# Performance work log

Hardware: AMD Instinct MI355X
Metric: run time of the kernel (lower is better)

Reference implementation:

```python
import jax, jax.numpy as jnp
import numpy as np

ANCHORS = [[[116, 90], [156, 198], [373, 326]], [[30, 61], [62, 45], [59, 119]], [[10, 13], [16, 30], [33, 23]]]
INPUT_SIZE = 416.0
B, G, C = 32, 20, 80


def _decode_scale(inp, anch):
    # inp: [B, 3*(5+C), W, W]
    Bq, _, W, _ = inp.shape
    sf = INPUT_SIZE / W
    p = inp.reshape(Bq, 3, -1, W, W).transpose(0, 1, 3, 4, 2)  # [B,3,W,W,5+C]
    sx = jax.nn.sigmoid(p[..., 0])
    sy = jax.nn.sigmoid(p[..., 1])
    w = p[..., 2]
    h = p[..., 3]
    conf = jax.nn.sigmoid(p[..., 4])
    cls = jax.nn.sigmoid(p[..., 5:])
    gx = jnp.arange(W, dtype=inp.dtype)[None, None, None, :]  # varies along cols
    gy = jnp.arange(W, dtype=inp.dtype)[None, None, :, None]  # varies along rows
    a = jnp.floor(jnp.asarray(anch, dtype=inp.dtype) / sf)  # // scale_factor as in source
    aw = a[:, 0][None, :, None, None]
    ah = a[:, 1][None, :, None, None]
    bx = (sx + gx) * sf
    by = (sy + gy) * sf
    bw = jnp.exp(w) * aw * sf
    bh = jnp.exp(h) * ah * sf
    out = jnp.concatenate([bx[..., None], by[..., None], bw[..., None], bh[..., None], conf[..., None], cls], axis=-1)
    return out.reshape(Bq, -1, 5 + cls.shape[-1])  # [B, 3*W*W, 5+C]


def _forward(x0, x1, x2, batch_y):
    xs = [x0, x1, x2]
    Bq = x0.shape[0]
    img_dim = x0.shape[1] // 3
    w1 = x0.shape[-1]  # source uses width1 for ALL scales (faithful bug reproduction)
    raw = jnp.concatenate(
        [xi.reshape(Bq, 3, -1, w1, w1).transpose(0, 1, 3, 4, 2).reshape(Bq, -1, img_dim) for xi in xs], axis=1)
    dec = jnp.concatenate([_decode_scale(xi, ANCHORS[i]) for i, xi in enumerate(xs)], axis=1)  # [B,N,5+C]
    # pairwise IoU between every decoded box [B,1,N] and every GT [B,G,1]
    pb = dec[..., :4]
    px, py, pw, ph = pb[..., 0][:, None, :], pb[..., 1][:, None, :], pb[..., 2][:, None, :], pb[..., 3][:, None, :]
    gb = batch_y[..., :4]
    gxc, gyc, gw, gh = gb[..., 0][..., None], gb[..., 1][..., None], gb[..., 2][..., None], gb[..., 3][..., None]
    xl = jnp.maximum(px, gxc)
    yt = jnp.maximum(py, gyc)
    xr = jnp.minimum(px + pw, gxc + gw)
    yb = jnp.minimum(py + ph, gyc + gh)
    inter = jnp.clip(xr - xl, 0) * jnp.clip(yb - yt, 0)
    iou = inter / (pw * ph + gw * gh - inter)  # [B,G,N]
    pos = jnp.argmax(iou, axis=-1)  # [B,G] (first max, like torch.max)
    neg_mask = (iou < 0.5).astype(dec.dtype)  # [B,G,N]
    x_pos = jnp.take_along_axis(raw[..., :4], pos[..., None], axis=1)  # [B,G,4]
    conf = dec[..., 4]  # [B,N]
    conf_pos = jnp.take_along_axis(conf, pos, axis=1)  # [B,G]
    cls_pos = jnp.take_along_axis(dec[..., 5:], pos[..., None], axis=1)  # [B,G,C]
    labels = batch_y[..., 4].astype(jnp.int32)  # [B,G]
    mse = jnp.mean((x_pos - gb) ** 2, axis=-1)  # MSELoss on the single matched row
    obj = jnp.log(conf_pos + 1e-9)
    log1m = jnp.log(1.0 - conf + 1e-9)[:, None, :]  # [B,1,N]
    cnt = jnp.maximum(jnp.sum(neg_mask, axis=-1), 1.0)
    noobj = jnp.sum(neg_mask * log1m, axis=-1) / cnt  # masked mean over negatives
    ce = -jnp.take_along_axis(jax.nn.log_softmax(cls_pos, axis=-1), labels[..., None], axis=-1)[..., 0]
    # loss += box*MSE - obj*mean(log conf) - noobj*mean(log(1-conf)) - class*CE  (rates all 1)
    return jnp.sum(1.0 * mse - 1.0 * obj - 1.0 * noobj - 1.0 * ce)


def setup_inputs() -> dict:
    key = jax.random.key(0)
    k0, k1, k2, k3, k4, k5 = jax.random.split(key, 6)
    ch = 3 * (5 + C)
    x0 = jax.random.normal(k0, (B, ch, 13, 13), dtype=jnp.float32)
    x1 = jax.random.normal(k1, (B, ch, 26, 26), dtype=jnp.float32)
    x2 = jax.random.normal(k2, (B, ch, 52, 52), dtype=jnp.float32)
    xy = jax.random.uniform(k3, (B, G, 2), dtype=jnp.float32) * 350.0
    wh = jax.random.uniform(k4, (B, G, 2), dtype=jnp.float32) * 90.0 + 10.0
    lab = jax.random.randint(k5, (B, G, 1), 0, C).astype(jnp.float32)
    batch_y = jnp.concatenate([xy, wh, lab], axis=-1)  # [B,G,5]: x,y,w,h,class
    return {"x0": x0, "x1": x1, "x2": x2, "batch_y": batch_y}


def reference(x0, x1, x2, batch_y):
    return _forward(x0, x1, x2, batch_y)
```

## Files before the change

kernel.cpp:

```cpp
#include <hip/hip_runtime.h>


constexpr int B_ = 32;
constexpr int G_ = 20;
constexpr int C_ = 80;

__global__ void zero_out_kernel(float* __restrict__ out) {
    out[0] = 0.0f;
}

__device__ __forceinline__ float sigm(float x) { return 1.0f / (1.0f + expf(-x)); }

template <int W, int NBASE>
__device__ __forceinline__ void scan_scale(
    const float* __restrict__ x, int b, float sf,
    float aw0, float aw1, float aw2, float ah0, float ah1, float ah2,
    float gxc, float gyc, float gx2, float gy2, float garea,
    float& best_iou, int& best_idx, float& neg_sum, float& neg_cnt)
{
    constexpr int WW = W * W;
    constexpr int NS = 3 * WW;
    for (int i = threadIdx.x; i < NS; i += 256) {
        int a   = i / WW;
        int rem = i - a * WW;
        int y   = rem / W;
        int xi  = rem - y * W;
        const float* base = x + (size_t)(b * 255 + a * 85) * WW + rem;
        float p0 = base[0];
        float p1 = base[WW];
        float p2 = base[2 * WW];
        float p3 = base[3 * WW];
        float p4 = base[4 * WW];
        float aw = (a == 0) ? aw0 : ((a == 1) ? aw1 : aw2);
        float ah = (a == 0) ? ah0 : ((a == 1) ? ah1 : ah2);
        float px = (sigm(p0) + (float)xi) * sf;
        float py = (sigm(p1) + (float)y) * sf;
        float pw = expf(p2) * aw;
        float ph = expf(p3) * ah;
        float conf = sigm(p4);
        float xl = fmaxf(px, gxc);
        float yt = fmaxf(py, gyc);
        float xr = fminf(px + pw, gx2);
        float yb = fminf(py + ph, gy2);
        float inter = fmaxf(xr - xl, 0.0f) * fmaxf(yb - yt, 0.0f);
        float iou = inter / (pw * ph + garea - inter);
        if (iou > best_iou) { best_iou = iou; best_idx = NBASE + i; }
        if (iou < 0.5f) { neg_sum += logf(1.0f - conf + 1e-9f); neg_cnt += 1.0f; }
    }
}

__global__ __launch_bounds__(256) void yolo_loss_kernel(
    const float* __restrict__ x0, const float* __restrict__ x1,
    const float* __restrict__ x2, const float* __restrict__ by,
    float* __restrict__ out)
{
    const int g = blockIdx.x;
    const int b = blockIdx.y;
    const float* yrow = by + (size_t)(b * G_ + g) * 5;
    const float gxc = yrow[0], gyc = yrow[1], gw = yrow[2], gh = yrow[3];
    const int label = (int)yrow[4];
    const float gx2 = gxc + gw, gy2 = gyc + gh, garea = gw * gh;

    float best_iou = -1e30f;
    int best_idx = 0x7fffffff;
    float neg_sum = 0.0f, neg_cnt = 0.0f;

    scan_scale<13, 0>(x0, b, 32.0f, 96.0f, 128.0f, 352.0f, 64.0f, 192.0f, 320.0f,
                      gxc, gyc, gx2, gy2, garea, best_iou, best_idx, neg_sum, neg_cnt);
    scan_scale<26, 507>(x1, b, 16.0f, 16.0f, 48.0f, 48.0f, 48.0f, 32.0f, 112.0f,
                        gxc, gyc, gx2, gy2, garea, best_iou, best_idx, neg_sum, neg_cnt);
    scan_scale<52, 2535>(x2, b, 8.0f, 8.0f, 16.0f, 32.0f, 8.0f, 24.0f, 16.0f,
                         gxc, gyc, gx2, gy2, garea, best_iou, best_idx, neg_sum, neg_cnt);

    for (int off = 32; off > 0; off >>= 1) {
        float oi  = __shfl_down(best_iou, off);
        int   oix = __shfl_down(best_idx, off);
        float ons = __shfl_down(neg_sum, off);
        float onc = __shfl_down(neg_cnt, off);
        if (oi > best_iou || (oi == best_iou && oix < best_idx)) { best_iou = oi; best_idx = oix; }
        neg_sum += ons;
        neg_cnt += onc;
    }

    __shared__ float s_iou[4];
    __shared__ int   s_idx[4];
    __shared__ float s_ns[4], s_nc[4];
    const int wave = threadIdx.x >> 6;
    const int lane = threadIdx.x & 63;
    if (lane == 0) { s_iou[wave] = best_iou; s_idx[wave] = best_idx; s_ns[wave] = neg_sum; s_nc[wave] = neg_cnt; }
    __syncthreads();

    if (threadIdx.x < 64) {
        float biou = (lane < 4) ? s_iou[lane] : -1e30f;
        int   bidx = (lane < 4) ? s_idx[lane] : 0x7fffffff;
        float ns   = (lane < 4) ? s_ns[lane] : 0.0f;
        float nc   = (lane < 4) ? s_nc[lane] : 0.0f;
        for (int off = 2; off > 0; off >>= 1) {
            float oi  = __shfl_xor(biou, off);
            int   oix = __shfl_xor(bidx, off);
            float ons = __shfl_xor(ns, off);
            float onc = __shfl_xor(nc, off);
            if (oi > biou || (oi == biou && oix < bidx)) { biou = oi; bidx = oix; }
            ns += ons;
            nc += onc;
        }
        const int pos = __shfl(bidx, 0);

        const float* xp;
        int local, WWv;
        if (pos < 507)        { xp = x0; local = pos;        WWv = 169;  }
        else if (pos < 2535)  { xp = x1; local = pos - 507;  WWv = 676;  }
        else                  { xp = x2; local = pos - 2535; WWv = 2704; }
        const int a   = local / WWv;
        const int rem = local - a * WWv;
        const float* basep = xp + (size_t)(b * 255 + a * 85) * WWv + rem;

        float s0v = sigm(basep[(5 + lane) * WWv]);
        float s1v = -1e30f;
        if (lane < C_ - 64) s1v = sigm(basep[(5 + 64 + lane) * WWv]);
        float m = fmaxf(s0v, s1v);
        for (int off = 32; off > 0; off >>= 1) m = fmaxf(m, __shfl_xor(m, off));
        float e = expf(s0v - m) + ((lane < C_ - 64) ? expf(s1v - m) : 0.0f);
        for (int off = 32; off > 0; off >>= 1) e += __shfl_xor(e, off);

        if (lane == 0) {
            float vl = sigm(basep[(5 + label) * WWv]);
            float ce = -(vl - m - logf(e));

            float r0 = basep[0];
            float r1 = basep[WWv];
            float r2 = basep[2 * WWv];
            float r3 = basep[3 * WWv];
            float d0 = r0 - gxc, d1 = r1 - gyc, d2 = r2 - gw, d3 = r3 - gh;
            float mse = 0.25f * (d0 * d0 + d1 * d1 + d2 * d2 + d3 * d3);

            float confp = sigm(basep[4 * WWv]);
            float obj = logf(confp + 1e-9f);
            float noobj = ns / fmaxf(nc, 1.0f);

            atomicAdd(out, mse - obj - noobj - ce);
        }
    }
}

extern "C" void kernel_launch(void* const* d_in, const int* in_sizes, int n_in,
                              void* d_out, int out_size, void* d_ws, size_t ws_size,
                              hipStream_t stream) {
    const float* x0 = (const float*)d_in[0];
    const float* x1 = (const float*)d_in[1];
    const float* x2 = (const float*)d_in[2];
    const float* by = (const float*)d_in[3];
    float* out = (float*)d_out;

    hipLaunchKernelGGL(zero_out_kernel, dim3(1), dim3(1), 0, stream, out);
    dim3 grid(G_, B_);
    hipLaunchKernelGGL(yolo_loss_kernel, grid, dim3(256), 0, stream,
                       x0, x1, x2, by, out);
}
```

Baseline: 181.4 us.

## Precompute decoded boxes once per batch and reuse across GT scans

Adds a decode kernel that computes box corners, area and log(1-conf) once per anchor per batch and writes them to workspace, plus a per-batch total of log1m. The scan kernel then reads the precomputed float4 pairs instead of redoing sigmoid/exp/log for every GT. The negative sum is obtained as the total minus the positive sum, which removes the per-GT log. The scan blocks are also remapped so that one batch's GTs share an XCD for L2 reuse. The cost is extra kernel launches and a workspace write and read of about 11 MB. The original path is kept as a fallback when the workspace is too small.

New measurement: 164.9 us. -9.1%, faster.

```diff
diff --git a/kernel.cpp b/kernel.cpp
--- a/kernel.cpp
+++ b/kernel.cpp
@@ -4,15 +4,202 @@
 constexpr int B_ = 32;
 constexpr int G_ = 20;
 constexpr int C_ = 80;
-
-__global__ void zero_out_kernel(float* __restrict__ out) {
-    out[0] = 0.0f;
-}
+constexpr int N_ = 10647;
+
+constexpr size_t DEC_BYTES = (size_t)B_ * N_ * 2 * sizeof(float4);
+constexpr size_t WS_NEEDED = DEC_BYTES + B_ * sizeof(float);
 
 __device__ __forceinline__ float sigm(float x) { return 1.0f / (1.0f + expf(-x)); }
 
+__global__ void init_kernel(float* __restrict__ tot, float* __restrict__ out) {
+    int t = threadIdx.x;
+    if (t < B_) tot[t] = 0.0f;
+    if (t == 0) out[0] = 0.0f;
+}
+
 template <int W, int NBASE>
-__device__ __forceinline__ void scan_scale(
+__device__ __forceinline__ void decode_scale(
+    const float* __restrict__ x, int b, int n, float sf,
+    float aw0, float aw1, float aw2, float ah0, float ah1, float ah2,
+    float4& d0, float4& d1)
+{
+    constexpr int WW = W * W;
+    int local = n - NBASE;
+    int a   = local / WW;
+    int rem = local - a * WW;
+    int y   = rem / W;
+    int xi  = rem - y * W;
+    const float* base = x + (size_t)(b * 255 + a * 85) * WW + rem;
+    float p0 = base[0];
+    float p1 = base[WW];
+    float p2 = base[2 * WW];
+    float p3 = base[3 * WW];
+    float p4 = base[4 * WW];
+    float aw = (a == 0) ? aw0 : ((a == 1) ? aw1 : aw2);
+    float ah = (a == 0) ? ah0 : ((a == 1) ? ah1 : ah2);
+    float px = (sigm(p0) + (float)xi) * sf;
+    float py = (sigm(p1) + (float)y) * sf;
+    float pw = expf(p2) * aw;
+    float ph = expf(p3) * ah;
+    float conf  = sigm(p4);
+    float log1m = logf(1.0f - conf + 1e-9f);
+    d0 = make_float4(px, py, px + pw, py + ph);
+    d1 = make_float4(pw * ph, log1m, 0.0f, 0.0f);
+}
+
+__global__ __launch_bounds__(256) void decode_kernel(
+    const float* __restrict__ x0, const float* __restrict__ x1,
+    const float* __restrict__ x2,
+    float4* __restrict__ dec, float* __restrict__ tot)
+{
+    const int b = blockIdx.y;
+    const int base = blockIdx.x * 1024;
+    float lsum = 0.0f;
+    for (int k = 0; k < 4; ++k) {
+        int n = base + k * 256 + threadIdx.x;
+        if (n < N_) {
+            float4 d0, d1;
+            if (n < 507)
+                decode_scale<13, 0>(x0, b, n, 32.0f, 96.0f, 128.0f, 352.0f,
+                                    64.0f, 192.0f, 320.0f, d0, d1);
+            else if (n < 2535)
+                decode_scale<26, 507>(x1, b, n, 16.0f, 16.0f, 48.0f, 48.0f,
+                                      48.0f, 32.0f, 112.0f, d0, d1);
+            else
+                decode_scale<52, 2535>(x2, b, n, 8.0f, 8.0f, 16.0f, 32.0f,
+                                       8.0f, 24.0f, 16.0f, d0, d1);
+            lsum += d1.y;
+            size_t o = ((size_t)b * N_ + n) * 2;
+            dec[o]     = d0;
+            dec[o + 1] = d1;
+        }
+    }
+    for (int off = 32; off > 0; off >>= 1) lsum += __shfl_down(lsum, off);
+    __shared__ float s_sum[4];
+    const int wave = threadIdx.x >> 6;
+    const int lane = threadIdx.x & 63;
+    if (lane == 0) s_sum[wave] = lsum;
+    __syncthreads();
+    if (threadIdx.x == 0)
+        atomicAdd(&tot[b], s_sum[0] + s_sum[1] + s_sum[2] + s_sum[3]);
+}
+
+__global__ __launch_bounds__(256) void scan_kernel(
+    const float* __restrict__ x0, const float* __restrict__ x1,
+    const float* __restrict__ x2,
+    const float4* __restrict__ dec, const float* __restrict__ by,
+    const float* __restrict__ tot, float* __restrict__ out)
+{
+    const int id   = blockIdx.x;
+    const int xcd  = id & 7;
+    const int slot = id >> 3;
+    const int q    = slot / 20;
+    const int b    = xcd * 4 + q;
+    const int g    = slot - q * 20;
+
+    const float* yrow = by + (size_t)(b * G_ + g) * 5;
+    const float gxc = yrow[0], gyc = yrow[1], gw = yrow[2], gh = yrow[3];
+    const int label = (int)yrow[4];
+    const float gx2 = gxc + gw, gy2 = gyc + gh, garea = gw * gh;
+
+    const float4* dp = dec + (size_t)b * N_ * 2;
+
+    float best_iou = -1.0f;
+    int best_idx = 0x7fffffff;
+    float pos_sum = 0.0f, pos_cnt = 0.0f;
+
+    for (int n = threadIdx.x; n < N_; n += 256) {
+        float4 d0 = dp[2 * n];
+        float4 d1 = dp[2 * n + 1];
+        float xl = fmaxf(d0.x, gxc);
+        float yt = fmaxf(d0.y, gyc);
+        float xr = fminf(d0.z, gx2);
+        float yb = fminf(d0.w, gy2);
+        float inter = fmaxf(xr - xl, 0.0f) * fmaxf(yb - yt, 0.0f);
+        float u = d1.x + garea - inter;
+        float iou = inter / u;
+        if (iou > best_iou) { best_iou = iou; best_idx = n; }
+        if (iou >= 0.5f) { pos_sum += d1.y; pos_cnt += 1.0f; }
+    }
+
+    for (int off = 32; off > 0; off >>= 1) {
+        float oi  = __shfl_down(best_iou, off);
+        int   oix = __shfl_down(best_idx, off);
+        float ops = __shfl_down(pos_sum, off);
+        float opc = __shfl_down(pos_cnt, off);
+        if (oi > best_iou || (oi == best_iou && oix < best_idx)) { best_iou = oi; best_idx = oix; }
+        pos_sum += ops;
+        pos_cnt += opc;
+    }
+
+    __shared__ float s_iou[4];
+    __shared__ int   s_idx[4];
+    __shared__ float s_ps[4], s_pc[4];
+    const int wave = threadIdx.x >> 6;
+    const int lane = threadIdx.x & 63;
+    if (lane == 0) { s_iou[wave] = best_iou; s_idx[wave] = best_idx; s_ps[wave] = pos_sum; s_pc[wave] = pos_cnt; }
+    __syncthreads();
+
+    if (threadIdx.x < 64) {
+        float biou = (lane < 4) ? s_iou[lane] : -1.0f;
+        int   bidx = (lane < 4) ? s_idx[lane] : 0x7fffffff;
+        float ps   = (lane < 4) ? s_ps[lane] : 0.0f;
+        float pc   = (lane < 4) ? s_pc[lane] : 0.0f;
+        for (int off = 2; off > 0; off >>= 1) {
+            float oi  = __shfl_xor(biou, off);
+            int   oix = __shfl_xor(bidx, off);
+            float ops = __shfl_xor(ps, off);
+            float opc = __shfl_xor(pc, off);
+            if (oi > biou || (oi == biou && oix < bidx)) { biou = oi; bidx = oix; }
+            ps += ops;
+            pc += opc;
+        }
+        const int pos = __shfl(bidx, 0);
+
+        const float* xp;
+        int local, WWv;
+        if (pos < 507)        { xp = x0; local = pos;        WWv = 169;  }
+        else if (pos < 2535)  { xp = x1; local = pos - 507;  WWv = 676;  }
+        else                  { xp = x2; local = pos - 2535; WWv = 2704; }
+        const int a   = local / WWv;
+        const int rem = local - a * WWv;
+        const float* basep = xp + (size_t)(b * 255 + a * 85) * WWv + rem;
+
+        float s0v = sigm(basep[(5 + lane) * WWv]);
+        float s1v = -1e30f;
+        if (lane < C_ - 64) s1v = sigm(basep[(5 + 64 + lane) * WWv]);
+        float m = fmaxf(s0v, s1v);
+        for (int off = 32; off > 0; off >>= 1) m = fmaxf(m, __shfl_xor(m, off));
+        float e = expf(s0v - m) + ((lane < C_ - 64) ? expf(s1v - m) : 0.0f);
+        for (int off = 32; off > 0; off >>= 1) e += __shfl_xor(e, off);
+
+        if (lane == 0) {
+            float vl = sigm(basep[(5 + label) * WWv]);
+            float ce = -(vl - m - logf(e));
+
+            float r0 = basep[0];
+            float r1 = basep[WWv];
+            float r2 = basep[2 * WWv];
+            float r3 = basep[3 * WWv];
+            float d0 = r0 - gxc, d1 = r1 - gyc, d2 = r2 - gw, d3 = r3 - gh;
+            float mse = 0.25f * (d0 * d0 + d1 * d1 + d2 * d2 + d3 * d3);
+
+            float confp = sigm(basep[4 * WWv]);
+            float obj = logf(confp + 1e-9f);
+
+            float neg_sum = tot[b] - ps;
+            float neg_cnt = (float)N_ - pc;
+            float noobj = neg_sum / fmaxf(neg_cnt, 1.0f);
+
+            atomicAdd(out, mse - obj - noobj - ce);
+        }
+    }
+}
+
+__global__ void zero_out_kernel(float* __restrict__ out) { out[0] = 0.0f; }
+
+template <int W, int NBASE>
+__device__ __forceinline__ void scan_scale_fb(
     const float* __restrict__ x, int b, float sf,
     float aw0, float aw1, float aw2, float ah0, float ah1, float ah2,
     float gxc, float gyc, float gx2, float gy2, float garea,
@@ -26,11 +213,7 @@
         int y   = rem / W;
         int xi  = rem - y * W;
         const float* base = x + (size_t)(b * 255 + a * 85) * WW + rem;
-        float p0 = base[0];
-        float p1 = base[WW];
-        float p2 = base[2 * WW];
-        float p3 = base[3 * WW];
-        float p4 = base[4 * WW];
+        float p0 = base[0], p1 = base[WW], p2 = base[2 * WW], p3 = base[3 * WW], p4 = base[4 * WW];
         float aw = (a == 0) ? aw0 : ((a == 1) ? aw1 : aw2);
         float ah = (a == 0) ? ah0 : ((a == 1) ? ah1 : ah2);
         float px = (sigm(p0) + (float)xi) * sf;
@@ -38,10 +221,8 @@
         float pw = expf(p2) * aw;
         float ph = expf(p3) * ah;
         float conf = sigm(p4);
-        float xl = fmaxf(px, gxc);
-        float yt = fmaxf(py, gyc);
-        float xr = fminf(px + pw, gx2);
-        float yb = fminf(py + ph, gy2);
+        float xl = fmaxf(px, gxc), yt = fmaxf(py, gyc);
+        float xr = fminf(px + pw, gx2), yb = fminf(py + ph, gy2);
         float inter = fmaxf(xr - xl, 0.0f) * fmaxf(yb - yt, 0.0f);
         float iou = inter / (pw * ph + garea - inter);
         if (iou > best_iou) { best_iou = iou; best_idx = NBASE + i; }
@@ -49,7 +230,7 @@
     }
 }
 
-__global__ __launch_bounds__(256) void yolo_loss_kernel(
+__global__ __launch_bounds__(256) void yolo_loss_fallback(
     const float* __restrict__ x0, const float* __restrict__ x1,
     const float* __restrict__ x2, const float* __restrict__ by,
     float* __restrict__ out)
@@ -65,12 +246,12 @@
     int best_idx = 0x7fffffff;
     float neg_sum = 0.0f, neg_cnt = 0.0f;
 
-    scan_scale<13, 0>(x0, b, 32.0f, 96.0f, 128.0f, 352.0f, 64.0f, 192.0f, 320.0f,
-                      gxc, gyc, gx2, gy2, garea, best_iou, best_idx, neg_sum, neg_cnt);
-    scan_scale<26, 507>(x1, b, 16.0f, 16.0f, 48.0f, 48.0f, 48.0f, 32.0f, 112.0f,
-                        gxc, gyc, gx2, gy2, garea, best_iou, best_idx, neg_sum, neg_cnt);
-    scan_scale<52, 2535>(x2, b, 8.0f, 8.0f, 16.0f, 32.0f, 8.0f, 24.0f, 16.0f,
+    scan_scale_fb<13, 0>(x0, b, 32.0f, 96.0f, 128.0f, 352.0f, 64.0f, 192.0f, 320.0f,
                          gxc, gyc, gx2, gy2, garea, best_iou, best_idx, neg_sum, neg_cnt);
+    scan_scale_fb<26, 507>(x1, b, 16.0f, 16.0f, 48.0f, 48.0f, 48.0f, 32.0f, 112.0f,
+                           gxc, gyc, gx2, gy2, garea, best_iou, best_idx, neg_sum, neg_cnt);
+    scan_scale_fb<52, 2535>(x2, b, 8.0f, 8.0f, 16.0f, 32.0f, 8.0f, 24.0f, 16.0f,
+                            gxc, gyc, gx2, gy2, garea, best_iou, best_idx, neg_sum, neg_cnt);
 
     for (int off = 32; off > 0; off >>= 1) {
         float oi  = __shfl_down(best_iou, off);
@@ -126,18 +307,12 @@
         if (lane == 0) {
             float vl = sigm(basep[(5 + label) * WWv]);
             float ce = -(vl - m - logf(e));
-
-            float r0 = basep[0];
-            float r1 = basep[WWv];
-            float r2 = basep[2 * WWv];
-            float r3 = basep[3 * WWv];
+            float r0 = basep[0], r1 = basep[WWv], r2 = basep[2 * WWv], r3 = basep[3 * WWv];
             float d0 = r0 - gxc, d1 = r1 - gyc, d2 = r2 - gw, d3 = r3 - gh;
             float mse = 0.25f * (d0 * d0 + d1 * d1 + d2 * d2 + d3 * d3);
-
             float confp = sigm(basep[4 * WWv]);
             float obj = logf(confp + 1e-9f);
             float noobj = ns / fmaxf(nc, 1.0f);
-
             atomicAdd(out, mse - obj - noobj - ce);
         }
     }
@@ -152,8 +327,17 @@
     const float* by = (const float*)d_in[3];
     float* out = (float*)d_out;
 
-    hipLaunchKernelGGL(zero_out_kernel, dim3(1), dim3(1), 0, stream, out);
-    dim3 grid(G_, B_);
-    hipLaunchKernelGGL(yolo_loss_kernel, grid, dim3(256), 0, stream,
-                       x0, x1, x2, by, out);
-}
+    if (ws_size >= WS_NEEDED) {
+        float4* dec = (float4*)d_ws;
+        float*  tot = (float*)((char*)d_ws + DEC_BYTES);
+        hipLaunchKernelGGL(init_kernel, dim3(1), dim3(64), 0, stream, tot, out);
+        hipLaunchKernelGGL(decode_kernel, dim3(11, B_), dim3(256), 0, stream,
+                           x0, x1, x2, dec, tot);
+        hipLaunchKernelGGL(scan_kernel, dim3(B_ * G_), dim3(256), 0, stream,
+                           x0, x1, x2, dec, by, tot, out);
+    } else {
+        hipLaunchKernelGGL(zero_out_kernel, dim3(1), dim3(1), 0, stream, out);
+        hipLaunchKernelGGL(yolo_loss_fallback, dim3(G_, B_), dim3(256), 0, stream,
+                           x0, x1, x2, by, out);
+    }
+}
```

## Decode boxes once per batch chunk and reuse across all GT boxes

Applied to the files above, without the earlier changes.

Previously every (batch, GT) block re-decoded all 10647 predicted boxes with sigmoid/exp/log, repeating the decode G times per batch. Now blocks tile over prediction chunks, decode each box once into registers, and loop over the 20 GT boxes held in shared memory. Argmax is merged across blocks with a packed 64-bit atomicMax key, and the negative-log sum is computed as total minus the positive sum. A separate epilogue kernel computes the per-GT loss terms. This adds workspace atomics and an extra launch, and the grid becomes small (6x32 blocks).

After: 168.9 us. 1.07x faster.

```diff
diff --git a/kernel.cpp b/kernel.cpp
--- a/kernel.cpp
+++ b/kernel.cpp
@@ -4,142 +4,213 @@
 constexpr int B_ = 32;
 constexpr int G_ = 20;
 constexpr int C_ = 80;
-
-__global__ void zero_out_kernel(float* __restrict__ out) {
-    out[0] = 0.0f;
-}
+constexpr int N_ = 10647;
+constexpr int PPT = 8;
+constexpr int CHUNK = 256 * PPT;
+constexpr int NCHUNK = (N_ + CHUNK - 1) / CHUNK;
+
+constexpr size_t OFF_KEY = 0;
+constexpr size_t OFF_PS  = OFF_KEY + (size_t)B_ * G_ * 8;
+constexpr size_t OFF_PC  = OFF_PS  + (size_t)B_ * G_ * 4;
+constexpr size_t OFF_TOT = OFF_PC  + (size_t)B_ * G_ * 4;
+constexpr size_t WS_NEEDED = OFF_TOT + B_ * 4;
 
 __device__ __forceinline__ float sigm(float x) { return 1.0f / (1.0f + expf(-x)); }
 
+__global__ __launch_bounds__(256) void init_kernel(
+    unsigned long long* __restrict__ key, float* __restrict__ ps,
+    float* __restrict__ pc, float* __restrict__ tot, float* __restrict__ out)
+{
+    const int t = threadIdx.x;
+    for (int i = t; i < B_ * G_; i += 256) { key[i] = 0ull; ps[i] = 0.0f; pc[i] = 0.0f; }
+    if (t < B_) tot[t] = 0.0f;
+    if (t == 0) out[0] = 0.0f;
+}
+
 template <int W, int NBASE>
-__device__ __forceinline__ void scan_scale(
-    const float* __restrict__ x, int b, float sf,
+__device__ __forceinline__ void decode_scale(
+    const float* __restrict__ x, int b, int n, float sf,
     float aw0, float aw1, float aw2, float ah0, float ah1, float ah2,
-    float gxc, float gyc, float gx2, float gy2, float garea,
-    float& best_iou, int& best_idx, float& neg_sum, float& neg_cnt)
+    float& x1o, float& y1o, float& x2o, float& y2o, float& area, float& l1m)
 {
     constexpr int WW = W * W;
-    constexpr int NS = 3 * WW;
-    for (int i = threadIdx.x; i < NS; i += 256) {
-        int a   = i / WW;
-        int rem = i - a * WW;
-        int y   = rem / W;
-        int xi  = rem - y * W;
-        const float* base = x + (size_t)(b * 255 + a * 85) * WW + rem;
-        float p0 = base[0];
-        float p1 = base[WW];
-        float p2 = base[2 * WW];
-        float p3 = base[3 * WW];
-        float p4 = base[4 * WW];
-        float aw = (a == 0) ? aw0 : ((a == 1) ? aw1 : aw2);
-        float ah = (a == 0) ? ah0 : ((a == 1) ? ah1 : ah2);
-        float px = (sigm(p0) + (float)xi) * sf;
-        float py = (sigm(p1) + (float)y) * sf;
-        float pw = expf(p2) * aw;
-        float ph = expf(p3) * ah;
-        float conf = sigm(p4);
-        float xl = fmaxf(px, gxc);
-        float yt = fmaxf(py, gyc);
-        float xr = fminf(px + pw, gx2);
-        float yb = fminf(py + ph, gy2);
-        float inter = fmaxf(xr - xl, 0.0f) * fmaxf(yb - yt, 0.0f);
-        float iou = inter / (pw * ph + garea - inter);
-        if (iou > best_iou) { best_iou = iou; best_idx = NBASE + i; }
-        if (iou < 0.5f) { neg_sum += logf(1.0f - conf + 1e-9f); neg_cnt += 1.0f; }
-    }
-}
-
-__global__ __launch_bounds__(256) void yolo_loss_kernel(
+    int local = n - NBASE;
+    int a   = local / WW;
+    int rem = local - a * WW;
+    int y   = rem / W;
+    int xi  = rem - y * W;
+    const float* base = x + (size_t)(b * 255 + a * 85) * WW + rem;
+    float p0 = base[0];
+    float p1 = base[WW];
+    float p2 = base[2 * WW];
+    float p3 = base[3 * WW];
+    float p4 = base[4 * WW];
+    float aw = (a == 0) ? aw0 : ((a == 1) ? aw1 : aw2);
+    float ah = (a == 0) ? ah0 : ((a == 1) ? ah1 : ah2);
+    float px = (sigm(p0) + (float)xi) * sf;
+    float py = (sigm(p1) + (float)y) * sf;
+    float pw = expf(p2) * aw;
+    float ph = expf(p3) * ah;
+    float conf = sigm(p4);
+    x1o = px; y1o = py; x2o = px + pw; y2o = py + ph;
+    area = pw * ph;
+    l1m = logf(1.0f - conf + 1e-9f);
+}
+
+__global__ __launch_bounds__(256) void fused_kernel(
     const float* __restrict__ x0, const float* __restrict__ x1,
     const float* __restrict__ x2, const float* __restrict__ by,
+    unsigned long long* __restrict__ key, float* __restrict__ ps,
+    float* __restrict__ pc, float* __restrict__ tot)
+{
+    const int b    = blockIdx.y;
+    const int base = blockIdx.x * CHUNK;
+    const int tid  = threadIdx.x;
+
+    __shared__ float s_gt[G_][5];
+    __shared__ unsigned long long s_key[G_][4];
+    __shared__ float s_ps[G_][4], s_pc[G_][4], s_l1m[4];
+
+    if (tid < G_) {
+        const float* yr = by + (size_t)(b * G_ + tid) * 5;
+        float gxc = yr[0], gyc = yr[1], gw = yr[2], gh = yr[3];
+        s_gt[tid][0] = gxc; s_gt[tid][1] = gyc;
+        s_gt[tid][2] = gxc + gw; s_gt[tid][3] = gyc + gh;
+        s_gt[tid][4] = gw * gh;
+    }
+    __syncthreads();
+
+    float bx1[PPT], by1[PPT], bx2[PPT], by2[PPT], bar[PPT], bl1[PPT];
+    float lsum = 0.0f;
+    #pragma unroll
+    for (int k = 0; k < PPT; ++k) {
+        int n = base + k * 256 + tid;
+        float X1 = 0, Y1 = 0, X2 = 0, Y2 = 0, AR = 0, L1 = 0;
+        if (n < N_) {
+            if (n < 507)
+                decode_scale<13, 0>(x0, b, n, 32.0f, 96.0f, 128.0f, 352.0f,
+                                    64.0f, 192.0f, 320.0f, X1, Y1, X2, Y2, AR, L1);
+            else if (n < 2535)
+                decode_scale<26, 507>(x1, b, n, 16.0f, 16.0f, 48.0f, 48.0f,
+                                      48.0f, 32.0f, 112.0f, X1, Y1, X2, Y2, AR, L1);
+            else
+                decode_scale<52, 2535>(x2, b, n, 8.0f, 8.0f, 16.0f, 32.0f,
+                                       8.0f, 24.0f, 16.0f, X1, Y1, X2, Y2, AR, L1);
+        }
+        bx1[k] = X1; by1[k] = Y1; bx2[k] = X2; by2[k] = Y2; bar[k] = AR; bl1[k] = L1;
+        lsum += L1;
+    }
+
+    const int wave = tid >> 6;
+    const int lane = tid & 63;
+    for (int g = 0; g < G_; ++g) {
+        float gxc = s_gt[g][0], gyc = s_gt[g][1];
+        float gx2 = s_gt[g][2], gy2 = s_gt[g][3], garea = s_gt[g][4];
+        float bi = -1.0f; int bidx = 0x7FFFFFFF;
+        float lps = 0.0f, lpc = 0.0f;
+        #pragma unroll
+        for (int k = 0; k < PPT; ++k) {
+            float xl = fmaxf(bx1[k], gxc);
+            float yt = fmaxf(by1[k], gyc);
+            float xr = fminf(bx2[k], gx2);
+            float yb = fminf(by2[k], gy2);
+            float inter = fmaxf(xr - xl, 0.0f) * fmaxf(yb - yt, 0.0f);
+            float u = bar[k] + garea - inter;
+            float iou = inter / u;
+            int n = base + k * 256 + tid;
+            iou = (n < N_) ? iou : -1.0f;
+            if (iou > bi) { bi = iou; bidx = n; }
+            if (iou >= 0.5f) { lps += bl1[k]; lpc += 1.0f; }
+        }
+        unsigned long long kk = (bi < 0.0f) ? 0ull
+            : (((unsigned long long)__float_as_uint(bi) << 32)
+               | (unsigned)(0x7FFFFFFF - bidx));
+        for (int off = 32; off > 0; off >>= 1) {
+            unsigned long long ok = __shfl_down(kk, off);
+            float ops = __shfl_down(lps, off);
+            float opc = __shfl_down(lpc, off);
+            kk = (ok > kk) ? ok : kk;
+            lps += ops; lpc += opc;
+        }
+        if (lane == 0) { s_key[g][wave] = kk; s_ps[g][wave] = lps; s_pc[g][wave] = lpc; }
+    }
+
+    for (int off = 32; off > 0; off >>= 1) lsum += __shfl_down(lsum, off);
+    if (lane == 0) s_l1m[wave] = lsum;
+    __syncthreads();
+
+    if (tid < G_) {
+        unsigned long long kk = s_key[tid][0];
+        float lps = s_ps[tid][0], lpc = s_pc[tid][0];
+        #pragma unroll
+        for (int w = 1; w < 4; ++w) {
+            unsigned long long ok = s_key[tid][w];
+            kk = (ok > kk) ? ok : kk;
+            lps += s_ps[tid][w]; lpc += s_pc[tid][w];
+        }
+        const int idx = b * G_ + tid;
+        atomicMax(&key[idx], kk);
+        atomicAdd(&ps[idx], lps);
+        atomicAdd(&pc[idx], lpc);
+    }
+    if (tid == 0)
+        atomicAdd(&tot[b], s_l1m[0] + s_l1m[1] + s_l1m[2] + s_l1m[3]);
+}
+
+__global__ __launch_bounds__(64) void epilogue_kernel(
+    const float* __restrict__ x0, const float* __restrict__ x1,
+    const float* __restrict__ x2, const float* __restrict__ by,
+    const unsigned long long* __restrict__ key, const float* __restrict__ ps,
+    const float* __restrict__ pc, const float* __restrict__ tot,
     float* __restrict__ out)
 {
     const int g = blockIdx.x;
     const int b = blockIdx.y;
+    const int lane = threadIdx.x;
+
+    const unsigned long long kk = key[b * G_ + g];
+    const int pos = 0x7FFFFFFF - (int)(kk & 0xFFFFFFFFull);
+
     const float* yrow = by + (size_t)(b * G_ + g) * 5;
     const float gxc = yrow[0], gyc = yrow[1], gw = yrow[2], gh = yrow[3];
     const int label = (int)yrow[4];
-    const float gx2 = gxc + gw, gy2 = gyc + gh, garea = gw * gh;
-
-    float best_iou = -1e30f;
-    int best_idx = 0x7fffffff;
-    float neg_sum = 0.0f, neg_cnt = 0.0f;
-
-    scan_scale<13, 0>(x0, b, 32.0f, 96.0f, 128.0f, 352.0f, 64.0f, 192.0f, 320.0f,
-                      gxc, gyc, gx2, gy2, garea, best_iou, best_idx, neg_sum, neg_cnt);
-    scan_scale<26, 507>(x1, b, 16.0f, 16.0f, 48.0f, 48.0f, 48.0f, 32.0f, 112.0f,
-                        gxc, gyc, gx2, gy2, garea, best_iou, best_idx, neg_sum, neg_cnt);
-    scan_scale<52, 2535>(x2, b, 8.0f, 8.0f, 16.0f, 32.0f, 8.0f, 24.0f, 16.0f,
-                         gxc, gyc, gx2, gy2, garea, best_iou, best_idx, neg_sum, neg_cnt);
-
-    for (int off = 32; off > 0; off >>= 1) {
-        float oi  = __shfl_down(best_iou, off);
-        int   oix = __shfl_down(best_idx, off);
-        float ons = __shfl_down(neg_sum, off);
-        float onc = __shfl_down(neg_cnt, off);
-        if (oi > best_iou || (oi == best_iou && oix < best_idx)) { best_iou = oi; best_idx = oix; }
-        neg_sum += ons;
-        neg_cnt += onc;
-    }
-
-    __shared__ float s_iou[4];
-    __shared__ int   s_idx[4];
-    __shared__ float s_ns[4], s_nc[4];
-    const int wave = threadIdx.x >> 6;
-    const int lane = threadIdx.x & 63;
-    if (lane == 0) { s_iou[wave] = best_iou; s_idx[wave] = best_idx; s_ns[wave] = neg_sum; s_nc[wave] = neg_cnt; }
-    __syncthreads();
-
-    if (threadIdx.x < 64) {
-        float biou = (lane < 4) ? s_iou[lane] : -1e30f;
-        int   bidx = (lane < 4) ? s_idx[lane] : 0x7fffffff;
-        float ns   = (lane < 4) ? s_ns[lane] : 0.0f;
-        float nc   = (lane < 4) ? s_nc[lane] : 0.0f;
-        for (int off = 2; off > 0; off >>= 1) {
-            float oi  = __shfl_xor(biou, off);
-            int   oix = __shfl_xor(bidx, off);
-            float ons = __shfl_xor(ns, off);
-            float onc = __shfl_xor(nc, off);
-            if (oi > biou || (oi == biou && oix < bidx)) { biou = oi; bidx = oix; }
-            ns += ons;
-            nc += onc;
-        }
-        const int pos = __shfl(bidx, 0);
-
-        const float* xp;
-        int local, WWv;
-        if (pos < 507)        { xp = x0; local = pos;        WWv = 169;  }
-        else if (pos < 2535)  { xp = x1; local = pos - 507;  WWv = 676;  }
-        else                  { xp = x2; local = pos - 2535; WWv = 2704; }
-        const int a   = local / WWv;
-        const int rem = local - a * WWv;
-        const float* basep = xp + (size_t)(b * 255 + a * 85) * WWv + rem;
-
-        float s0v = sigm(basep[(5 + lane) * WWv]);
-        float s1v = -1e30f;
-        if (lane < C_ - 64) s1v = sigm(basep[(5 + 64 + lane) * WWv]);
-        float m = fmaxf(s0v, s1v);
-        for (int off = 32; off > 0; off >>= 1) m = fmaxf(m, __shfl_xor(m, off));
-        float e = expf(s0v - m) + ((lane < C_ - 64) ? expf(s1v - m) : 0.0f);
-        for (int off = 32; off > 0; off >>= 1) e += __shfl_xor(e, off);
-
-        if (lane == 0) {
-            float vl = sigm(basep[(5 + label) * WWv]);
-            float ce = -(vl - m - logf(e));
-
-            float r0 = basep[0];
-            float r1 = basep[WWv];
-            float r2 = basep[2 * WWv];
-            float r3 = basep[3 * WWv];
-            float d0 = r0 - gxc, d1 = r1 - gyc, d2 = r2 - gw, d3 = r3 - gh;
-            float mse = 0.25f * (d0 * d0 + d1 * d1 + d2 * d2 + d3 * d3);
-
-            float confp = sigm(basep[4 * WWv]);
-            float obj = logf(confp + 1e-9f);
-            float noobj = ns / fmaxf(nc, 1.0f);
-
-            atomicAdd(out, mse - obj - noobj - ce);
-        }
+
+    const float* xp;
+    int local, WWv;
+    if (pos < 507)        { xp = x0; local = pos;        WWv = 169;  }
+    else if (pos < 2535)  { xp = x1; local = pos - 507;  WWv = 676;  }
+    else                  { xp = x2; local = pos - 2535; WWv = 2704; }
+    const int a   = local / WWv;
+    const int rem = local - a * WWv;
+    const float* basep = xp + (size_t)(b * 255 + a * 85) * WWv + rem;
+
+    float s0v = sigm(basep[(5 + lane) * WWv]);
+    float s1v = -1e30f;
+    if (lane < C_ - 64) s1v = sigm(basep[(5 + 64 + lane) * WWv]);
+    float m = fmaxf(s0v, s1v);
+    for (int off = 32; off > 0; off >>= 1) m = fmaxf(m, __shfl_xor(m, off));
+    float e = expf(s0v - m) + ((lane < C_ - 64) ? expf(s1v - m) : 0.0f);
+    for (int off = 32; off > 0; off >>= 1) e += __shfl_xor(e, off);
+
+    if (lane == 0) {
+        float vl = sigm(basep[(5 + label) * WWv]);
+        float ce = -(vl - m - logf(e));
+
+        float r0 = basep[0];
+        float r1 = basep[WWv];
+        float r2 = basep[2 * WWv];
+        float r3 = basep[3 * WWv];
+        float d0 = r0 - gxc, d1 = r1 - gyc, d2 = r2 - gw, d3 = r3 - gh;
+        float mse = 0.25f * (d0 * d0 + d1 * d1 + d2 * d2 + d3 * d3);
+
+        float confp = sigm(basep[4 * WWv]);
+        float obj = logf(confp + 1e-9f);
+
+        float neg_sum = tot[b] - ps[b * G_ + g];
+        float neg_cnt = (float)N_ - pc[b * G_ + g];
+        float noobj = neg_sum / fmaxf(neg_cnt, 1.0f);
+
+        atomicAdd(out, mse - obj - noobj - ce);
     }
 }
 
@@ -152,8 +223,15 @@
     const float* by = (const float*)d_in[3];
     float* out = (float*)d_out;
 
-    hipLaunchKernelGGL(zero_out_kernel, dim3(1), dim3(1), 0, stream, out);
-    dim3 grid(G_, B_);
-    hipLaunchKernelGGL(yolo_loss_kernel, grid, dim3(256), 0, stream,
-                       x0, x1, x2, by, out);
-}
+    unsigned long long* key = (unsigned long long*)((char*)d_ws + OFF_KEY);
+    float* ps  = (float*)((char*)d_ws + OFF_PS);
+    float* pc  = (float*)((char*)d_ws + OFF_PC);
+    float* tot = (float*)((char*)d_ws + OFF_TOT);
+
+    hipLaunchKernelGGL(init_kernel, dim3(1), dim3(256), 0, stream,
+                       key, ps, pc, tot, out);
+    hipLaunchKernelGGL(fused_kernel, dim3(NCHUNK, B_), dim3(256), 0, stream,
+                       x0, x1, x2, by, key, ps, pc, tot);
+    hipLaunchKernelGGL(epilogue_kernel, dim3(G_, B_), dim3(64), 0, stream,
+                       x0, x1, x2, by, key, ps, pc, tot, out);
+}
```
